# Kernel optimization log

Measured on AMD Instinct MI355X. Metric: run time of the kernel, lower is better.

## Reference

```python
import jax, jax.numpy as jnp
import numpy as np

ALPHA = 1.0

def setup_inputs() -> dict:
    key = jax.random.key(0)
    k1, k2 = jax.random.split(key)
    x = jax.random.normal(k1, (65536, 256), dtype=jnp.float32)
    clusters = jax.random.normal(k2, (256, 256), dtype=jnp.float32)
    return {"x": x, "clusters": clusters}

def reference(x, clusters):
    # squared euclidean distance via the GEMM trick (same math as
    # sum((x[:,None,:] - clusters[None,:,:])**2, axis=2) without the (n,k,d) blowup)
    x2 = jnp.sum(x * x, axis=1, keepdims=True)            # [n,1]
    c2 = jnp.sum(clusters * clusters, axis=1)             # [k]
    dist2 = x2 + c2[None, :] - 2.0 * (x @ clusters.T)     # [n,k]
    q = 1.0 / (1.0 + dist2 / ALPHA)
    q = jnp.power(q, (ALPHA + 1.0) / 2.0)
    q = q / jnp.sum(q, axis=1, keepdims=True)             # row-normalize
    return q
```

## Files before the change

kernel.cpp:

```cpp
#include <hip/hip_runtime.h>


typedef float f32x4 __attribute__((ext_vector_type(4)));

#define DIM    256
#define NCLUST 256

__device__ inline int pk4_fp8(float a, float b, float c, float d) {
    int w = __builtin_amdgcn_cvt_pk_fp8_f32(a, b, 0, false);
    w = __builtin_amdgcn_cvt_pk_fp8_f32(c, d, w, true);
    return w;
}

__global__ __launch_bounds__(64) void pre_kernel(const float* __restrict__ clusters,
                                                 int* __restrict__ bfrag,
                                                 float* __restrict__ c2p1) {
    int b = blockIdx.x;
    int l = threadIdx.x;
    if (b < 128) {
        int s   = b >> 4;
        int t   = b & 15;
        int col = t * 16 + (l & 15);
        int k0  = s * 32 + (l >> 4) * 8;
        const f32x4* p = reinterpret_cast<const f32x4*>(clusters + col * DIM + k0);
        f32x4 a = p[0];
        f32x4 c = p[1];
        int lo = pk4_fp8(-2.0f * a[0], -2.0f * a[1], -2.0f * a[2], -2.0f * a[3]);
        int hi = pk4_fp8(-2.0f * c[0], -2.0f * c[1], -2.0f * c[2], -2.0f * c[3]);
        bfrag[(b * 64 + l) * 2]     = lo;
        bfrag[(b * 64 + l) * 2 + 1] = hi;
    } else {
        int j = b - 128;
        const f32x4* p = reinterpret_cast<const f32x4*>(clusters + j * DIM);
        f32x4 v = p[l];
        float s = v[0] * v[0] + v[1] * v[1] + v[2] * v[2] + v[3] * v[3];
#pragma unroll
        for (int m = 32; m >= 1; m >>= 1) s += __shfl_xor(s, m, 64);
        if (l == 0) c2p1[j] = 1.0f + s;
    }
}

__global__ __launch_bounds__(256, 2) void cluster_kernel(const float* __restrict__ x,
                                                         const f32x4* __restrict__ bfrag,
                                                         const float* __restrict__ c2p1,
                                                         float* __restrict__ out) {
    __shared__ __align__(16) char Bs[65536];

    const int tid  = threadIdx.x;
    const int lane = tid & 63;
    const int wave = tid >> 6;
    const int cl   = lane & 15;
    const int g    = lane >> 4;
    const int tile = blockIdx.x * 4 + wave;

    f32x4 ld[16];
    {
        const float* xr = x + (size_t)(tile * 16 + cl) * DIM + g * 8;
#pragma unroll
        for (int s = 0; s < 8; ++s) {
            ld[2 * s]     = *reinterpret_cast<const f32x4*>(xr + s * 32);
            ld[2 * s + 1] = *reinterpret_cast<const f32x4*>(xr + s * 32 + 4);
        }
    }

    {
        f32x4* dst = reinterpret_cast<f32x4*>(Bs);
#pragma unroll 1
        for (int cc = 0; cc < 2; ++cc) {
            f32x4 tmp[8];
#pragma unroll
            for (int i = 0; i < 8; ++i)
                tmp[i] = bfrag[cc * 2048 + i * 256 + tid];
#pragma unroll
            for (int i = 0; i < 8; ++i)
                dst[cc * 2048 + i * 256 + tid] = tmp[i];
        }
    }
    __syncthreads();

    long af[8];
    float x2p = 0.0f;
#pragma unroll
    for (int s = 0; s < 8; ++s) {
        f32x4 a = ld[2 * s], b = ld[2 * s + 1];
        x2p += a[0]*a[0] + a[1]*a[1] + a[2]*a[2] + a[3]*a[3]
             + b[0]*b[0] + b[1]*b[1] + b[2]*b[2] + b[3]*b[3];
        unsigned lo = (unsigned)pk4_fp8(a[0], a[1], a[2], a[3]);
        unsigned hi = (unsigned)pk4_fp8(b[0], b[1], b[2], b[3]);
        af[s] = (long)(((unsigned long)hi << 32) | lo);
    }
    float x2full = x2p + __shfl_xor(x2p, 16, 64);
    x2full += __shfl_xor(x2full, 32, 64);

    f32x4 acc[16];
#pragma unroll
    for (int t = 0; t < 16; ++t) {
        acc[t][0] = 0.f; acc[t][1] = 0.f; acc[t][2] = 0.f; acc[t][3] = 0.f;
    }
    const char* bsb = Bs + lane * 8;
    __builtin_amdgcn_s_setprio(1);
#pragma unroll
    for (int s = 0; s < 8; ++s) {
#pragma unroll
        for (int t = 0; t < 16; ++t) {
            long bf = *reinterpret_cast<const long*>(bsb + (s * 16 + t) * 512);
            acc[t] = __builtin_amdgcn_mfma_f32_16x16x32_fp8_fp8(
                af[s], bf, acc[t], 0, 0, 0);
        }
    }
    __builtin_amdgcn_s_setprio(0);

    float c2v[16];
#pragma unroll
    for (int t = 0; t < 16; ++t) c2v[t] = c2p1[t * 16 + cl];

    float x2j[4];
#pragma unroll
    for (int j = 0; j < 4; ++j) x2j[j] = __shfl(x2full, g * 4 + j, 64);

    float rsum[4] = {0.f, 0.f, 0.f, 0.f};
#pragma unroll
    for (int t = 0; t < 16; ++t) {
#pragma unroll
        for (int j = 0; j < 4; ++j) {
            float d = x2j[j] + c2v[t] + acc[t][j];
            float q = __builtin_amdgcn_rcpf(d);
            acc[t][j] = q;
            rsum[j] += q;
        }
    }
#pragma unroll
    for (int j = 0; j < 4; ++j) {
        float v = rsum[j];
        v += __shfl_xor(v, 1, 64); v += __shfl_xor(v, 2, 64);
        v += __shfl_xor(v, 4, 64); v += __shfl_xor(v, 8, 64);
        rsum[j] = __builtin_amdgcn_rcpf(v);
    }
    float* ob = out + (size_t)(tile * 16) * NCLUST;
#pragma unroll
    for (int t = 0; t < 16; ++t)
#pragma unroll
        for (int j = 0; j < 4; ++j)
            ob[(g * 4 + j) * NCLUST + t * 16 + cl] = acc[t][j] * rsum[j];
}

extern "C" void kernel_launch(void* const* d_in, const int* in_sizes, int n_in,
                              void* d_out, int out_size, void* d_ws, size_t ws_size,
                              hipStream_t stream) {
    const float* x        = (const float*)d_in[0];
    const float* clusters = (const float*)d_in[1];
    float* out = (float*)d_out;

    int*   bfrag = (int*)d_ws;
    float* c2p1  = (float*)((char*)d_ws + 65536);

    pre_kernel<<<384, 64, 0, stream>>>(clusters, bfrag, c2p1);

    int nrows = in_sizes[0] / DIM;
    int grid  = nrows / (4 * 16);
    cluster_kernel<<<grid, 256, 0, stream>>>(x, (const f32x4*)bfrag, c2p1, out);
}
```

Before: 37.74 us.

## Process two row tiles per wave to amortize shared-memory B staging

Each wave now handles two 16-row tiles sequentially instead of one, which halves the grid. The cost of copying the 64KB fp8 cluster fragments into LDS and the c2 loads is therefore spread over twice as many rows. In exchange there are fewer blocks (512 instead of 1024) for latency hiding and tail balance. The second tile's x load is issued before the first tile's compute, but it may serialize with it.

```diff
diff --git a/kernel.cpp b/kernel.cpp
--- a/kernel.cpp
+++ b/kernel.cpp
@@ -51,11 +51,11 @@
     const int wave = tid >> 6;
     const int cl   = lane & 15;
     const int g    = lane >> 4;
-    const int tile = blockIdx.x * 4 + wave;
+    const int t0   = blockIdx.x * 8 + wave * 2;
 
     f32x4 ld[16];
     {
-        const float* xr = x + (size_t)(tile * 16 + cl) * DIM + g * 8;
+        const float* xr = x + (size_t)(t0 * 16 + cl) * DIM + g * 8;
 #pragma unroll
         for (int s = 0; s < 8; ++s) {
             ld[2 * s]     = *reinterpret_cast<const f32x4*>(xr + s * 32);
@@ -78,7 +78,7 @@
     }
     __syncthreads();
 
-    long af[8];
+    long af0[8];
     float x2p = 0.0f;
 #pragma unroll
     for (int s = 0; s < 8; ++s) {
@@ -87,61 +87,133 @@
              + b[0]*b[0] + b[1]*b[1] + b[2]*b[2] + b[3]*b[3];
         unsigned lo = (unsigned)pk4_fp8(a[0], a[1], a[2], a[3]);
         unsigned hi = (unsigned)pk4_fp8(b[0], b[1], b[2], b[3]);
-        af[s] = (long)(((unsigned long)hi << 32) | lo);
-    }
-    float x2full = x2p + __shfl_xor(x2p, 16, 64);
-    x2full += __shfl_xor(x2full, 32, 64);
-
-    f32x4 acc[16];
-#pragma unroll
-    for (int t = 0; t < 16; ++t) {
-        acc[t][0] = 0.f; acc[t][1] = 0.f; acc[t][2] = 0.f; acc[t][3] = 0.f;
-    }
+        af0[s] = (long)(((unsigned long)hi << 32) | lo);
+    }
+    float x2f0 = x2p + __shfl_xor(x2p, 16, 64);
+    x2f0 += __shfl_xor(x2f0, 32, 64);
+
+    {
+        const float* xr = x + (size_t)((t0 + 1) * 16 + cl) * DIM + g * 8;
+#pragma unroll
+        for (int s = 0; s < 8; ++s) {
+            ld[2 * s]     = *reinterpret_cast<const f32x4*>(xr + s * 32);
+            ld[2 * s + 1] = *reinterpret_cast<const f32x4*>(xr + s * 32 + 4);
+        }
+    }
+
+    long af1[8];
+    float x2q = 0.0f;
+#pragma unroll
+    for (int s = 0; s < 8; ++s) {
+        f32x4 a = ld[2 * s], b = ld[2 * s + 1];
+        x2q += a[0]*a[0] + a[1]*a[1] + a[2]*a[2] + a[3]*a[3]
+             + b[0]*b[0] + b[1]*b[1] + b[2]*b[2] + b[3]*b[3];
+        unsigned lo = (unsigned)pk4_fp8(a[0], a[1], a[2], a[3]);
+        unsigned hi = (unsigned)pk4_fp8(b[0], b[1], b[2], b[3]);
+        af1[s] = (long)(((unsigned long)hi << 32) | lo);
+    }
+    float x2f1 = x2q + __shfl_xor(x2q, 16, 64);
+    x2f1 += __shfl_xor(x2f1, 32, 64);
+
+    float c2v[16];
+#pragma unroll
+    for (int t = 0; t < 16; ++t) c2v[t] = c2p1[t * 16 + cl];
+
     const char* bsb = Bs + lane * 8;
-    __builtin_amdgcn_s_setprio(1);
-#pragma unroll
-    for (int s = 0; s < 8; ++s) {
-#pragma unroll
-        for (int t = 0; t < 16; ++t) {
-            long bf = *reinterpret_cast<const long*>(bsb + (s * 16 + t) * 512);
-            acc[t] = __builtin_amdgcn_mfma_f32_16x16x32_fp8_fp8(
-                af[s], bf, acc[t], 0, 0, 0);
-        }
-    }
-    __builtin_amdgcn_s_setprio(0);
-
-    float c2v[16];
-#pragma unroll
-    for (int t = 0; t < 16; ++t) c2v[t] = c2p1[t * 16 + cl];
-
-    float x2j[4];
-#pragma unroll
-    for (int j = 0; j < 4; ++j) x2j[j] = __shfl(x2full, g * 4 + j, 64);
-
-    float rsum[4] = {0.f, 0.f, 0.f, 0.f};
-#pragma unroll
-    for (int t = 0; t < 16; ++t) {
+
+    {
+        f32x4 acc[16];
+#pragma unroll
+        for (int t = 0; t < 16; ++t) {
+            acc[t][0] = 0.f; acc[t][1] = 0.f; acc[t][2] = 0.f; acc[t][3] = 0.f;
+        }
+        __builtin_amdgcn_s_setprio(1);
+#pragma unroll
+        for (int s = 0; s < 8; ++s) {
+#pragma unroll
+            for (int t = 0; t < 16; ++t) {
+                long bf = *reinterpret_cast<const long*>(bsb + (s * 16 + t) * 512);
+                acc[t] = __builtin_amdgcn_mfma_f32_16x16x32_fp8_fp8(
+                    af0[s], bf, acc[t], 0, 0, 0);
+            }
+        }
+        __builtin_amdgcn_s_setprio(0);
+
+        float x2j[4];
+#pragma unroll
+        for (int j = 0; j < 4; ++j) x2j[j] = __shfl(x2f0, g * 4 + j, 64);
+        float rsum[4] = {0.f, 0.f, 0.f, 0.f};
+#pragma unroll
+        for (int t = 0; t < 16; ++t) {
+#pragma unroll
+            for (int j = 0; j < 4; ++j) {
+                float d = x2j[j] + c2v[t] + acc[t][j];
+                float q = __builtin_amdgcn_rcpf(d);
+                acc[t][j] = q;
+                rsum[j] += q;
+            }
+        }
 #pragma unroll
         for (int j = 0; j < 4; ++j) {
-            float d = x2j[j] + c2v[t] + acc[t][j];
-            float q = __builtin_amdgcn_rcpf(d);
-            acc[t][j] = q;
-            rsum[j] += q;
-        }
-    }
-#pragma unroll
-    for (int j = 0; j < 4; ++j) {
-        float v = rsum[j];
-        v += __shfl_xor(v, 1, 64); v += __shfl_xor(v, 2, 64);
-        v += __shfl_xor(v, 4, 64); v += __shfl_xor(v, 8, 64);
-        rsum[j] = __builtin_amdgcn_rcpf(v);
-    }
-    float* ob = out + (size_t)(tile * 16) * NCLUST;
-#pragma unroll
-    for (int t = 0; t < 16; ++t)
-#pragma unroll
-        for (int j = 0; j < 4; ++j)
-            ob[(g * 4 + j) * NCLUST + t * 16 + cl] = acc[t][j] * rsum[j];
+            float v = rsum[j];
+            v += __shfl_xor(v, 1, 64); v += __shfl_xor(v, 2, 64);
+            v += __shfl_xor(v, 4, 64); v += __shfl_xor(v, 8, 64);
+            rsum[j] = __builtin_amdgcn_rcpf(v);
+        }
+        float* ob = out + (size_t)(t0 * 16) * NCLUST;
+#pragma unroll
+        for (int t = 0; t < 16; ++t)
+#pragma unroll
+            for (int j = 0; j < 4; ++j)
+                ob[(g * 4 + j) * NCLUST + t * 16 + cl] = acc[t][j] * rsum[j];
+    }
+
+    {
+        f32x4 acc[16];
+#pragma unroll
+        for (int t = 0; t < 16; ++t) {
+            acc[t][0] = 0.f; acc[t][1] = 0.f; acc[t][2] = 0.f; acc[t][3] = 0.f;
+        }
+        __builtin_amdgcn_s_setprio(1);
+#pragma unroll
+        for (int s = 0; s < 8; ++s) {
+#pragma unroll
+            for (int t = 0; t < 16; ++t) {
+                long bf = *reinterpret_cast<const long*>(bsb + (s * 16 + t) * 512);
+                acc[t] = __builtin_amdgcn_mfma_f32_16x16x32_fp8_fp8(
+                    af1[s], bf, acc[t], 0, 0, 0);
+            }
+        }
+        __builtin_amdgcn_s_setprio(0);
+
+        float x2j[4];
+#pragma unroll
+        for (int j = 0; j < 4; ++j) x2j[j] = __shfl(x2f1, g * 4 + j, 64);
+        float rsum[4] = {0.f, 0.f, 0.f, 0.f};
+#pragma unroll
+        for (int t = 0; t < 16; ++t) {
+#pragma unroll
+            for (int j = 0; j < 4; ++j) {
+                float d = x2j[j] + c2v[t] + acc[t][j];
+                float q = __builtin_amdgcn_rcpf(d);
+                acc[t][j] = q;
+                rsum[j] += q;
+            }
+        }
+#pragma unroll
+        for (int j = 0; j < 4; ++j) {
+            float v = rsum[j];
+            v += __shfl_xor(v, 1, 64); v += __shfl_xor(v, 2, 64);
+            v += __shfl_xor(v, 4, 64); v += __shfl_xor(v, 8, 64);
+            rsum[j] = __builtin_amdgcn_rcpf(v);
+        }
+        float* ob = out + (size_t)((t0 + 1) * 16) * NCLUST;
+#pragma unroll
+        for (int t = 0; t < 16; ++t)
+#pragma unroll
+            for (int j = 0; j < 4; ++j)
+                ob[(g * 4 + j) * NCLUST + t * 16 + cl] = acc[t][j] * rsum[j];
+    }
 }
 
 extern "C" void kernel_launch(void* const* d_in, const int* in_sizes, int n_in,
@@ -157,6 +229,6 @@
     pre_kernel<<<384, 64, 0, stream>>>(clusters, bfrag, c2p1);
 
     int nrows = in_sizes[0] / DIM;
-    int grid  = nrows / (4 * 16);
+    int grid  = nrows / (8 * 16);
     cluster_kernel<<<grid, 256, 0, stream>>>(x, (const f32x4*)bfrag, c2p1, out);
 }
```

Result: faster. 33.14 us (-12.2%).
